# Performance work log

Hardware: AMD Instinct MI355X
Metric: run time of the kernel (lower is better)

Reference implementation:

```python
import jax, jax.numpy as jnp
import numpy as np

HEADS, BATCH, SEQ, CDIM = 8, 4, 2048, 32
WINDOW = 10

def setup_inputs() -> dict:
    key = jax.random.key(0)
    k1, k2, k3, k4 = jax.random.split(key, 4)
    shp = (HEADS, BATCH, SEQ, CDIM)
    return {
        'Q': jax.random.normal(k1, shp, dtype=jnp.float32),
        'K': jax.random.normal(k2, shp, dtype=jnp.float32),
        'V': jax.random.normal(k3, shp, dtype=jnp.float32),
        'G': jax.random.normal(k4, shp, dtype=jnp.float32),
        'seqMask': jnp.zeros((BATCH, SEQ), dtype=bool),  # no padded positions
    }

def reference(Q, K, V, G, seqMask):
    # Q,K,V,G: [h, n, s, c]; seqMask: [n, s] bool (True = masked key position)
    scale = 1.0 / jnp.sqrt(jnp.asarray(CDIM, dtype=Q.dtype))
    A = jnp.einsum('hnsi,hnti->hnst', Q, K) * scale  # [h,n,s,t]
    # padding mask on key axis
    A = jnp.where(seqMask[None, :, None, :], -jnp.inf, A)
    # local band mask |s-t| <= WINDOW (torch scatter construction clamps to
    # row bounds, which is equivalent to the plain band)
    idx = jnp.arange(SEQ)
    band = jnp.abs(idx[:, None] - idx[None, :]) <= WINDOW  # [s,t]
    A = jnp.where(band[None, None, :, :], A, -jnp.inf)
    A = jax.nn.softmax(A, axis=-1)
    # gated AV fusion: out[n,s,h,i] = sum_t A[h,n,s,t] V[h,n,t,i] * G[h,n,s,i]
    out = jnp.einsum('hnst,hnti,hnsi->nshi', A, V, G)
    return out
```

## Files before the change

### kernel.cpp

```cpp
#include <hip/hip_runtime.h>
#include <hip/hip_bf16.h>
#include <math.h>

#define HEADS 8
#define BATCH 4
#define SEQ 2048
#define CDIM 32
#define WINDOW 10

#define RPB 64
#define VROWS 96
#define VSTR 20

typedef float f32x4 __attribute__((ext_vector_type(4)));
typedef short s16x8 __attribute__((ext_vector_type(8)));
#define MFMA16 __builtin_amdgcn_mfma_f32_16x16x32_bf16

union BF8 { s16x8 v; __hip_bfloat162 h[4]; };
union U32 { __hip_bfloat162 h; unsigned u; };
union U4  { unsigned u[4]; s16x8 v; };

__global__ __launch_bounds__(256) void lwin_attn_kernel(
    const float* __restrict__ Q, const float* __restrict__ K,
    const float* __restrict__ V, const float* __restrict__ G,
    const unsigned char* __restrict__ seqMask, float* __restrict__ out)
{
    __shared__ unsigned V_s[VROWS * VSTR];

    const int d = blockIdx.x;
    const int b = (d & 7) * 128 + (d >> 3);

    const int hn = b >> 5;
    const int s0 = (b & 31) * RPB;
    const int n  = hn & 3;
    const int h  = hn >> 2;
    const int base_hn = hn * SEQ * CDIM;

    const int tid  = threadIdx.x;
    const int w    = tid >> 6;
    const int lane = tid & 63;
    const int q    = lane & 15;
    const int g    = lane >> 4;

    {
        const int i = tid >> 2, o = tid & 3;
        const int t  = s0 - 16 + i;
        const int tc = min(max(t, 0), SEQ - 1);
        const float4 f0 = *(const float4*)&V[base_hn + tc * 32 + 4 * o];
        const float4 f1 = *(const float4*)&V[base_hn + tc * 32 + 16 + 4 * o];
        U32 w0, w1, w2, w3;
        w0.h = __float22bfloat162_rn(make_float2(f0.x, f1.x));
        w1.h = __float22bfloat162_rn(make_float2(f0.y, f1.y));
        w2.h = __float22bfloat162_rn(make_float2(f0.z, f1.z));
        w3.h = __float22bfloat162_rn(make_float2(f0.w, f1.w));
        *(uint4*)&V_s[i * VSTR + 4 * o] = make_uint4(w0.u, w1.u, w2.u, w3.u);
    }
    if (tid < 128) {
        const int task = tid + 256;
        const int i = task >> 2, o = task & 3;
        const int t  = s0 - 16 + i;
        const int tc = min(max(t, 0), SEQ - 1);
        const float4 f0 = *(const float4*)&V[base_hn + tc * 32 + 4 * o];
        const float4 f1 = *(const float4*)&V[base_hn + tc * 32 + 16 + 4 * o];
        U32 w0, w1, w2, w3;
        w0.h = __float22bfloat162_rn(make_float2(f0.x, f1.x));
        w1.h = __float22bfloat162_rn(make_float2(f0.y, f1.y));
        w2.h = __float22bfloat162_rn(make_float2(f0.z, f1.z));
        w3.h = __float22bfloat162_rn(make_float2(f0.w, f1.w));
        *(uint4*)&V_s[i * VSTR + 4 * o] = make_uint4(w0.u, w1.u, w2.u, w3.u);
    }

    const int sw = s0 + 16 * w;

    const int rowq = hn * SEQ + sw + q;
    const float sc = 0.17677669529663687f * 1.4426950408889634f;
    const float4 q0 = *(const float4*)&Q[rowq * 32 + 8 * g];
    const float4 q1 = *(const float4*)&Q[rowq * 32 + 8 * g + 4];
    BF8 bq;
    bq.h[0] = __float22bfloat162_rn(make_float2(q0.x * sc, q0.y * sc));
    bq.h[1] = __float22bfloat162_rn(make_float2(q0.z * sc, q0.w * sc));
    bq.h[2] = __float22bfloat162_rn(make_float2(q1.x * sc, q1.y * sc));
    bq.h[3] = __float22bfloat162_rn(make_float2(q1.z * sc, q1.w * sc));
    const float4 g0 = *(const float4*)&G[rowq * 32 + 4 * g];
    const float4 g1 = *(const float4*)&G[rowq * 32 + 16 + 4 * g];

    BF8 ak[3];
#pragma unroll
    for (int blk = 0; blk < 3; ++blk) {
        const int t  = sw - 16 + 16 * blk + q;
        const int tc = min(max(t, 0), SEQ - 1);
        const float4 k0 = *(const float4*)&K[base_hn + tc * 32 + 8 * g];
        const float4 k1 = *(const float4*)&K[base_hn + tc * 32 + 8 * g + 4];
        ak[blk].h[0] = __float22bfloat162_rn(make_float2(k0.x, k0.y));
        ak[blk].h[1] = __float22bfloat162_rn(make_float2(k0.z, k0.w));
        ak[blk].h[2] = __float22bfloat162_rn(make_float2(k1.x, k1.y));
        ak[blk].h[3] = __float22bfloat162_rn(make_float2(k1.z, k1.w));
    }

    unsigned long long mI;
    {
        const int t  = sw - 16 + lane;
        const int tc = min(max(t, 0), SEQ - 1);
        const bool inval = (t < 0) || (t >= SEQ) || (seqMask[n * SEQ + tc] != 0);
        mI = __ballot(inval);
    }
    const unsigned long long vm = (0x1FFFFFULL << (q + 6)) & ~mI;

    f32x4 S[3];
#pragma unroll
    for (int blk = 0; blk < 3; ++blk)
        S[blk] = MFMA16(ak[blk].v, bq.v, (f32x4){0.f, 0.f, 0.f, 0.f}, 0, 0, 0);

    float sm = 0.f;
    unsigned pk[3][2];
#pragma unroll
    for (int blk = 0; blk < 3; ++blk) {
        float e[4];
#pragma unroll
        for (int r = 0; r < 4; ++r) {
            const int j = 16 * blk + 4 * g + r;
            const float x = ((vm >> j) & 1ULL) ? S[blk][r] : -1e30f;
            e[r] = __builtin_amdgcn_exp2f(x);
            sm += e[r];
        }
        U32 a, b2;
        a.h  = __float22bfloat162_rn(make_float2(e[0], e[1]));
        b2.h = __float22bfloat162_rn(make_float2(e[2], e[3]));
        pk[blk][0] = a.u;
        pk[blk][1] = b2.u;
    }
    sm += __shfl_xor(sm, 16);
    sm += __shfl_xor(sm, 32);

    __syncthreads();

    f32x4 O0 = {0.f, 0.f, 0.f, 0.f}, O1 = {0.f, 0.f, 0.f, 0.f};
    {
        const int R = 16 * w;
        unsigned r0[4], r1[4];
#pragma unroll
        for (int jj = 0; jj < 4; ++jj) {
            r0[jj] = V_s[(R + 4 * g + jj) * VSTR + q];
            r1[jj] = V_s[(R + 16 + 4 * g + jj) * VSTR + q];
        }
        U4 A0, A1v;
        A0.u[0]  = __builtin_amdgcn_perm(r0[1], r0[0], 0x05040100u);
        A0.u[1]  = __builtin_amdgcn_perm(r0[3], r0[2], 0x05040100u);
        A0.u[2]  = __builtin_amdgcn_perm(r1[1], r1[0], 0x05040100u);
        A0.u[3]  = __builtin_amdgcn_perm(r1[3], r1[2], 0x05040100u);
        A1v.u[0] = __builtin_amdgcn_perm(r0[1], r0[0], 0x07060302u);
        A1v.u[1] = __builtin_amdgcn_perm(r0[3], r0[2], 0x07060302u);
        A1v.u[2] = __builtin_amdgcn_perm(r1[1], r1[0], 0x07060302u);
        A1v.u[3] = __builtin_amdgcn_perm(r1[3], r1[2], 0x07060302u);
        U4 Bp;
        Bp.u[0] = pk[0][0]; Bp.u[1] = pk[0][1];
        Bp.u[2] = pk[1][0]; Bp.u[3] = pk[1][1];
        O0 = MFMA16(A0.v,  Bp.v, O0, 0, 0, 0);
        O1 = MFMA16(A1v.v, Bp.v, O1, 0, 0, 0);
    }
    {
        const int R = 16 * w + 32;
        unsigned r0[4];
#pragma unroll
        for (int jj = 0; jj < 4; ++jj)
            r0[jj] = V_s[(R + 4 * g + jj) * VSTR + q];
        U4 A0, A1v;
        A0.u[0]  = __builtin_amdgcn_perm(r0[1], r0[0], 0x05040100u);
        A0.u[1]  = __builtin_amdgcn_perm(r0[3], r0[2], 0x05040100u);
        A0.u[2]  = 0u; A0.u[3] = 0u;
        A1v.u[0] = __builtin_amdgcn_perm(r0[1], r0[0], 0x07060302u);
        A1v.u[1] = __builtin_amdgcn_perm(r0[3], r0[2], 0x07060302u);
        A1v.u[2] = 0u; A1v.u[3] = 0u;
        U4 Bp;
        Bp.u[0] = pk[2][0]; Bp.u[1] = pk[2][1];
        Bp.u[2] = 0u;       Bp.u[3] = 0u;
        O0 = MFMA16(A0.v,  Bp.v, O0, 0, 0, 0);
        O1 = MFMA16(A1v.v, Bp.v, O1, 0, 0, 0);
    }

    const float invq = 1.0f / sm;
    float4 o0, o1;
    o0.x = O0[0] * invq * g0.x;  o0.y = O0[1] * invq * g0.y;
    o0.z = O0[2] * invq * g0.z;  o0.w = O0[3] * invq * g0.w;
    o1.x = O1[0] * invq * g1.x;  o1.y = O1[1] * invq * g1.y;
    o1.z = O1[2] * invq * g1.z;  o1.w = O1[3] * invq * g1.w;
    float* obase = &out[((n * SEQ + sw + q) * HEADS + h) * 32];
    *(float4*)&obase[4 * g]      = o0;
    *(float4*)&obase[16 + 4 * g] = o1;
}

extern "C" void kernel_launch(void* const* d_in, const int* in_sizes, int n_in,
                              void* d_out, int out_size, void* d_ws, size_t ws_size,
                              hipStream_t stream) {
    const float* Q = (const float*)d_in[0];
    const float* K = (const float*)d_in[1];
    const float* V = (const float*)d_in[2];
    const float* G = (const float*)d_in[3];
    const unsigned char* seqMask = (const unsigned char*)d_in[4];
    float* out = (float*)d_out;

    const int blocks = HEADS * BATCH * (SEQ / RPB);
    lwin_attn_kernel<<<blocks, 256, 0, stream>>>(Q, K, V, G, seqMask, out);
}
```

Measured before the change: 14.17 us.

## Split channel halves across wave pairs and stage bf16 K in shared memory

Each block now covers 32 query rows instead of 64. Pairs of waves share one 16-row tile, and each wave computes one 16-channel half of the output, so the block count doubles and each wave does half the AV work. K is converted to bf16 once per block and staged in LDS, replacing the per-wave global loads of overlapping K windows. The trade-off is that QK^T and softmax are computed redundantly in both waves of a pair, and there is more halo overhead per block.

```diff
diff --git a/kernel.cpp b/kernel.cpp
--- a/kernel.cpp
+++ b/kernel.cpp
@@ -8,8 +8,8 @@
 #define CDIM 32
 #define WINDOW 10
 
-#define RPB 64
-#define VROWS 96
+#define RPB 32
+#define BROWS 64
 #define VSTR 20
 
 typedef float f32x4 __attribute__((ext_vector_type(4)));
@@ -25,19 +25,22 @@
     const float* __restrict__ V, const float* __restrict__ G,
     const unsigned char* __restrict__ seqMask, float* __restrict__ out)
 {
-    __shared__ unsigned V_s[VROWS * VSTR];
+    __shared__ short    K_s[BROWS * 32];
+    __shared__ unsigned V_s[BROWS * VSTR];
 
     const int d = blockIdx.x;
-    const int b = (d & 7) * 128 + (d >> 3);
+    const int b = (d & 7) * 256 + (d >> 3);
 
-    const int hn = b >> 5;
-    const int s0 = (b & 31) * RPB;
+    const int hn = b >> 6;
+    const int s0 = (b & 63) * RPB;
     const int n  = hn & 3;
     const int h  = hn >> 2;
     const int base_hn = hn * SEQ * CDIM;
 
     const int tid  = threadIdx.x;
-    const int w    = tid >> 6;
+    const int wave = tid >> 6;
+    const int tile = wave >> 1;
+    const int half = wave & 1;
     const int lane = tid & 63;
     const int q    = lane & 15;
     const int g    = lane >> 4;
@@ -46,22 +49,16 @@
         const int i = tid >> 2, o = tid & 3;
         const int t  = s0 - 16 + i;
         const int tc = min(max(t, 0), SEQ - 1);
+        const float4 k0 = *(const float4*)&K[base_hn + tc * 32 + 8 * o];
+        const float4 k1 = *(const float4*)&K[base_hn + tc * 32 + 8 * o + 4];
         const float4 f0 = *(const float4*)&V[base_hn + tc * 32 + 4 * o];
         const float4 f1 = *(const float4*)&V[base_hn + tc * 32 + 16 + 4 * o];
-        U32 w0, w1, w2, w3;
-        w0.h = __float22bfloat162_rn(make_float2(f0.x, f1.x));
-        w1.h = __float22bfloat162_rn(make_float2(f0.y, f1.y));
-        w2.h = __float22bfloat162_rn(make_float2(f0.z, f1.z));
-        w3.h = __float22bfloat162_rn(make_float2(f0.w, f1.w));
-        *(uint4*)&V_s[i * VSTR + 4 * o] = make_uint4(w0.u, w1.u, w2.u, w3.u);
-    }
-    if (tid < 128) {
-        const int task = tid + 256;
-        const int i = task >> 2, o = task & 3;
-        const int t  = s0 - 16 + i;
-        const int tc = min(max(t, 0), SEQ - 1);
-        const float4 f0 = *(const float4*)&V[base_hn + tc * 32 + 4 * o];
-        const float4 f1 = *(const float4*)&V[base_hn + tc * 32 + 16 + 4 * o];
+        BF8 uk;
+        uk.h[0] = __float22bfloat162_rn(make_float2(k0.x, k0.y));
+        uk.h[1] = __float22bfloat162_rn(make_float2(k0.z, k0.w));
+        uk.h[2] = __float22bfloat162_rn(make_float2(k1.x, k1.y));
+        uk.h[3] = __float22bfloat162_rn(make_float2(k1.z, k1.w));
+        *(s16x8*)&K_s[i * 32 + 8 * o] = uk.v;
         U32 w0, w1, w2, w3;
         w0.h = __float22bfloat162_rn(make_float2(f0.x, f1.x));
         w1.h = __float22bfloat162_rn(make_float2(f0.y, f1.y));
@@ -70,9 +67,9 @@
         *(uint4*)&V_s[i * VSTR + 4 * o] = make_uint4(w0.u, w1.u, w2.u, w3.u);
     }
 
-    const int sw = s0 + 16 * w;
+    const int sw   = s0 + 16 * tile;
+    const int rowq = hn * SEQ + sw + q;
 
-    const int rowq = hn * SEQ + sw + q;
     const float sc = 0.17677669529663687f * 1.4426950408889634f;
     const float4 q0 = *(const float4*)&Q[rowq * 32 + 8 * g];
     const float4 q1 = *(const float4*)&Q[rowq * 32 + 8 * g + 4];
@@ -81,21 +78,7 @@
     bq.h[1] = __float22bfloat162_rn(make_float2(q0.z * sc, q0.w * sc));
     bq.h[2] = __float22bfloat162_rn(make_float2(q1.x * sc, q1.y * sc));
     bq.h[3] = __float22bfloat162_rn(make_float2(q1.z * sc, q1.w * sc));
-    const float4 g0 = *(const float4*)&G[rowq * 32 + 4 * g];
-    const float4 g1 = *(const float4*)&G[rowq * 32 + 16 + 4 * g];
-
-    BF8 ak[3];
-#pragma unroll
-    for (int blk = 0; blk < 3; ++blk) {
-        const int t  = sw - 16 + 16 * blk + q;
-        const int tc = min(max(t, 0), SEQ - 1);
-        const float4 k0 = *(const float4*)&K[base_hn + tc * 32 + 8 * g];
-        const float4 k1 = *(const float4*)&K[base_hn + tc * 32 + 8 * g + 4];
-        ak[blk].h[0] = __float22bfloat162_rn(make_float2(k0.x, k0.y));
-        ak[blk].h[1] = __float22bfloat162_rn(make_float2(k0.z, k0.w));
-        ak[blk].h[2] = __float22bfloat162_rn(make_float2(k1.x, k1.y));
-        ak[blk].h[3] = __float22bfloat162_rn(make_float2(k1.z, k1.w));
-    }
+    const float4 gh = *(const float4*)&G[rowq * 32 + 16 * half + 4 * g];
 
     unsigned long long mI;
     {
@@ -106,10 +89,14 @@
     }
     const unsigned long long vm = (0x1FFFFFULL << (q + 6)) & ~mI;
 
+    __syncthreads();
+
     f32x4 S[3];
 #pragma unroll
-    for (int blk = 0; blk < 3; ++blk)
-        S[blk] = MFMA16(ak[blk].v, bq.v, (f32x4){0.f, 0.f, 0.f, 0.f}, 0, 0, 0);
+    for (int blk = 0; blk < 3; ++blk) {
+        const s16x8 ak = *(const s16x8*)&K_s[(16 * tile + 16 * blk + q) * 32 + 8 * g];
+        S[blk] = MFMA16(ak, bq.v, (f32x4){0.f, 0.f, 0.f, 0.f}, 0, 0, 0);
+    }
 
     float sm = 0.f;
     unsigned pk[3][2];
@@ -132,61 +119,47 @@
     sm += __shfl_xor(sm, 16);
     sm += __shfl_xor(sm, 32);
 
-    __syncthreads();
-
-    f32x4 O0 = {0.f, 0.f, 0.f, 0.f}, O1 = {0.f, 0.f, 0.f, 0.f};
+    const unsigned sel = half ? 0x07060302u : 0x05040100u;
+    f32x4 O = {0.f, 0.f, 0.f, 0.f};
     {
-        const int R = 16 * w;
+        const int R = 16 * tile;
         unsigned r0[4], r1[4];
 #pragma unroll
         for (int jj = 0; jj < 4; ++jj) {
             r0[jj] = V_s[(R + 4 * g + jj) * VSTR + q];
             r1[jj] = V_s[(R + 16 + 4 * g + jj) * VSTR + q];
         }
-        U4 A0, A1v;
-        A0.u[0]  = __builtin_amdgcn_perm(r0[1], r0[0], 0x05040100u);
-        A0.u[1]  = __builtin_amdgcn_perm(r0[3], r0[2], 0x05040100u);
-        A0.u[2]  = __builtin_amdgcn_perm(r1[1], r1[0], 0x05040100u);
-        A0.u[3]  = __builtin_amdgcn_perm(r1[3], r1[2], 0x05040100u);
-        A1v.u[0] = __builtin_amdgcn_perm(r0[1], r0[0], 0x07060302u);
-        A1v.u[1] = __builtin_amdgcn_perm(r0[3], r0[2], 0x07060302u);
-        A1v.u[2] = __builtin_amdgcn_perm(r1[1], r1[0], 0x07060302u);
-        A1v.u[3] = __builtin_amdgcn_perm(r1[3], r1[2], 0x07060302u);
+        U4 A;
+        A.u[0] = __builtin_amdgcn_perm(r0[1], r0[0], sel);
+        A.u[1] = __builtin_amdgcn_perm(r0[3], r0[2], sel);
+        A.u[2] = __builtin_amdgcn_perm(r1[1], r1[0], sel);
+        A.u[3] = __builtin_amdgcn_perm(r1[3], r1[2], sel);
         U4 Bp;
         Bp.u[0] = pk[0][0]; Bp.u[1] = pk[0][1];
         Bp.u[2] = pk[1][0]; Bp.u[3] = pk[1][1];
-        O0 = MFMA16(A0.v,  Bp.v, O0, 0, 0, 0);
-        O1 = MFMA16(A1v.v, Bp.v, O1, 0, 0, 0);
+        O = MFMA16(A.v, Bp.v, O, 0, 0, 0);
     }
     {
-        const int R = 16 * w + 32;
+        const int R = 16 * tile + 32;
         unsigned r0[4];
 #pragma unroll
         for (int jj = 0; jj < 4; ++jj)
             r0[jj] = V_s[(R + 4 * g + jj) * VSTR + q];
-        U4 A0, A1v;
-        A0.u[0]  = __builtin_amdgcn_perm(r0[1], r0[0], 0x05040100u);
-        A0.u[1]  = __builtin_amdgcn_perm(r0[3], r0[2], 0x05040100u);
-        A0.u[2]  = 0u; A0.u[3] = 0u;
-        A1v.u[0] = __builtin_amdgcn_perm(r0[1], r0[0], 0x07060302u);
-        A1v.u[1] = __builtin_amdgcn_perm(r0[3], r0[2], 0x07060302u);
-        A1v.u[2] = 0u; A1v.u[3] = 0u;
+        U4 A;
+        A.u[0] = __builtin_amdgcn_perm(r0[1], r0[0], sel);
+        A.u[1] = __builtin_amdgcn_perm(r0[3], r0[2], sel);
+        A.u[2] = 0u; A.u[3] = 0u;
         U4 Bp;
         Bp.u[0] = pk[2][0]; Bp.u[1] = pk[2][1];
         Bp.u[2] = 0u;       Bp.u[3] = 0u;
-        O0 = MFMA16(A0.v,  Bp.v, O0, 0, 0, 0);
-        O1 = MFMA16(A1v.v, Bp.v, O1, 0, 0, 0);
+        O = MFMA16(A.v, Bp.v, O, 0, 0, 0);
     }
 
     const float invq = 1.0f / sm;
-    float4 o0, o1;
-    o0.x = O0[0] * invq * g0.x;  o0.y = O0[1] * invq * g0.y;
-    o0.z = O0[2] * invq * g0.z;  o0.w = O0[3] * invq * g0.w;
-    o1.x = O1[0] * invq * g1.x;  o1.y = O1[1] * invq * g1.y;
-    o1.z = O1[2] * invq * g1.z;  o1.w = O1[3] * invq * g1.w;
-    float* obase = &out[((n * SEQ + sw + q) * HEADS + h) * 32];
-    *(float4*)&obase[4 * g]      = o0;
-    *(float4*)&obase[16 + 4 * g] = o1;
+    float4 o;
+    o.x = O[0] * invq * gh.x;  o.y = O[1] * invq * gh.y;
+    o.z = O[2] * invq * gh.z;  o.w = O[3] * invq * gh.w;
+    *(float4*)&out[((n * SEQ + sw + q) * HEADS + h) * 32 + 16 * half + 4 * g] = o;
 }
 
 extern "C" void kernel_launch(void* const* d_in, const int* in_sizes, int n_in,
```

After: 12.94 us. 8.7% less time.

## Process two 64-row phases per block with staged K/V shared-memory double buffering

Applied to the files above, without the earlier changes.

Each block now covers 128 query rows in two 64-row phases and is launched half as many times. All global loads for both phases (K, V, Q, G, mask) are issued up front into registers. K is also staged through shared memory in bf16, alongside V, in a double-buffered layout so phase two's commit can follow phase one's compute. The aim is to cut per-block launch overhead and hide global latency, at the cost of more registers, lower occupancy, and a still-redundant 32-row halo per phase.

```diff
diff --git a/kernel.cpp b/kernel.cpp
--- a/kernel.cpp
+++ b/kernel.cpp
@@ -8,8 +8,8 @@
 #define CDIM 32
 #define WINDOW 10
 
-#define RPB 64
-#define VROWS 96
+#define RPB 128
+#define PBAND 96
 #define VSTR 20
 
 typedef float f32x4 __attribute__((ext_vector_type(4)));
@@ -25,13 +25,14 @@
     const float* __restrict__ V, const float* __restrict__ G,
     const unsigned char* __restrict__ seqMask, float* __restrict__ out)
 {
-    __shared__ unsigned V_s[VROWS * VSTR];
+    __shared__ short    K_s[2][PBAND * 32];
+    __shared__ unsigned V_s[2][PBAND * VSTR];
 
     const int d = blockIdx.x;
-    const int b = (d & 7) * 128 + (d >> 3);
-
-    const int hn = b >> 5;
-    const int s0 = (b & 31) * RPB;
+    const int b = (d & 7) * 64 + (d >> 3);
+
+    const int hn = b >> 4;
+    const int s0 = (b & 15) * RPB;
     const int n  = hn & 3;
     const int h  = hn >> 2;
     const int base_hn = hn * SEQ * CDIM;
@@ -42,151 +43,166 @@
     const int q    = lane & 15;
     const int g    = lane >> 4;
 
-    {
-        const int i = tid >> 2, o = tid & 3;
-        const int t  = s0 - 16 + i;
-        const int tc = min(max(t, 0), SEQ - 1);
-        const float4 f0 = *(const float4*)&V[base_hn + tc * 32 + 4 * o];
-        const float4 f1 = *(const float4*)&V[base_hn + tc * 32 + 16 + 4 * o];
-        U32 w0, w1, w2, w3;
-        w0.h = __float22bfloat162_rn(make_float2(f0.x, f1.x));
-        w1.h = __float22bfloat162_rn(make_float2(f0.y, f1.y));
-        w2.h = __float22bfloat162_rn(make_float2(f0.z, f1.z));
-        w3.h = __float22bfloat162_rn(make_float2(f0.w, f1.w));
-        *(uint4*)&V_s[i * VSTR + 4 * o] = make_uint4(w0.u, w1.u, w2.u, w3.u);
+    float4 ld[2][3][2];
+#pragma unroll
+    for (int p = 0; p < 2; ++p) {
+        const int sp = s0 + 64 * p;
+#pragma unroll
+        for (int k = 0; k < 3; ++k) {
+            const int id = tid + 256 * k;
+            const bool isK = id < 384;
+            const int tt = isK ? id : id - 384;
+            const int i = tt >> 2, o = tt & 3;
+            const int t  = sp - 16 + i;
+            const int tc = min(max(t, 0), SEQ - 1);
+            const float* src = (isK ? K : V) + base_hn + tc * 32;
+            const int off0 = isK ? 8 * o : 4 * o;
+            const int off1 = isK ? 8 * o + 4 : 16 + 4 * o;
+            ld[p][k][0] = *(const float4*)&src[off0];
+            ld[p][k][1] = *(const float4*)&src[off1];
+        }
     }
-    if (tid < 128) {
-        const int task = tid + 256;
-        const int i = task >> 2, o = task & 3;
-        const int t  = s0 - 16 + i;
-        const int tc = min(max(t, 0), SEQ - 1);
-        const float4 f0 = *(const float4*)&V[base_hn + tc * 32 + 4 * o];
-        const float4 f1 = *(const float4*)&V[base_hn + tc * 32 + 16 + 4 * o];
-        U32 w0, w1, w2, w3;
-        w0.h = __float22bfloat162_rn(make_float2(f0.x, f1.x));
-        w1.h = __float22bfloat162_rn(make_float2(f0.y, f1.y));
-        w2.h = __float22bfloat162_rn(make_float2(f0.z, f1.z));
-        w3.h = __float22bfloat162_rn(make_float2(f0.w, f1.w));
-        *(uint4*)&V_s[i * VSTR + 4 * o] = make_uint4(w0.u, w1.u, w2.u, w3.u);
-    }
-
-    const int sw = s0 + 16 * w;
-
-    const int rowq = hn * SEQ + sw + q;
+
     const float sc = 0.17677669529663687f * 1.4426950408889634f;
-    const float4 q0 = *(const float4*)&Q[rowq * 32 + 8 * g];
-    const float4 q1 = *(const float4*)&Q[rowq * 32 + 8 * g + 4];
-    BF8 bq;
-    bq.h[0] = __float22bfloat162_rn(make_float2(q0.x * sc, q0.y * sc));
-    bq.h[1] = __float22bfloat162_rn(make_float2(q0.z * sc, q0.w * sc));
-    bq.h[2] = __float22bfloat162_rn(make_float2(q1.x * sc, q1.y * sc));
-    bq.h[3] = __float22bfloat162_rn(make_float2(q1.z * sc, q1.w * sc));
-    const float4 g0 = *(const float4*)&G[rowq * 32 + 4 * g];
-    const float4 g1 = *(const float4*)&G[rowq * 32 + 16 + 4 * g];
-
-    BF8 ak[3];
-#pragma unroll
-    for (int blk = 0; blk < 3; ++blk) {
-        const int t  = sw - 16 + 16 * blk + q;
-        const int tc = min(max(t, 0), SEQ - 1);
-        const float4 k0 = *(const float4*)&K[base_hn + tc * 32 + 8 * g];
-        const float4 k1 = *(const float4*)&K[base_hn + tc * 32 + 8 * g + 4];
-        ak[blk].h[0] = __float22bfloat162_rn(make_float2(k0.x, k0.y));
-        ak[blk].h[1] = __float22bfloat162_rn(make_float2(k0.z, k0.w));
-        ak[blk].h[2] = __float22bfloat162_rn(make_float2(k1.x, k1.y));
-        ak[blk].h[3] = __float22bfloat162_rn(make_float2(k1.z, k1.w));
-    }
-
-    unsigned long long mI;
-    {
+    BF8 bq[2];
+    float4 gA[2], gB[2];
+    unsigned long long mI[2];
+#pragma unroll
+    for (int p = 0; p < 2; ++p) {
+        const int sw   = s0 + 64 * p + 16 * w;
+        const int rowq = hn * SEQ + sw + q;
+        const float4 q0 = *(const float4*)&Q[rowq * 32 + 8 * g];
+        const float4 q1 = *(const float4*)&Q[rowq * 32 + 8 * g + 4];
+        bq[p].h[0] = __float22bfloat162_rn(make_float2(q0.x * sc, q0.y * sc));
+        bq[p].h[1] = __float22bfloat162_rn(make_float2(q0.z * sc, q0.w * sc));
+        bq[p].h[2] = __float22bfloat162_rn(make_float2(q1.x * sc, q1.y * sc));
+        bq[p].h[3] = __float22bfloat162_rn(make_float2(q1.z * sc, q1.w * sc));
+        gA[p] = *(const float4*)&G[rowq * 32 + 4 * g];
+        gB[p] = *(const float4*)&G[rowq * 32 + 16 + 4 * g];
         const int t  = sw - 16 + lane;
         const int tc = min(max(t, 0), SEQ - 1);
         const bool inval = (t < 0) || (t >= SEQ) || (seqMask[n * SEQ + tc] != 0);
-        mI = __ballot(inval);
+        mI[p] = __ballot(inval);
     }
-    const unsigned long long vm = (0x1FFFFFULL << (q + 6)) & ~mI;
-
-    f32x4 S[3];
-#pragma unroll
-    for (int blk = 0; blk < 3; ++blk)
-        S[blk] = MFMA16(ak[blk].v, bq.v, (f32x4){0.f, 0.f, 0.f, 0.f}, 0, 0, 0);
-
-    float sm = 0.f;
-    unsigned pk[3][2];
-#pragma unroll
-    for (int blk = 0; blk < 3; ++blk) {
-        float e[4];
-#pragma unroll
-        for (int r = 0; r < 4; ++r) {
-            const int j = 16 * blk + 4 * g + r;
-            const float x = ((vm >> j) & 1ULL) ? S[blk][r] : -1e30f;
-            e[r] = __builtin_amdgcn_exp2f(x);
-            sm += e[r];
-        }
-        U32 a, b2;
-        a.h  = __float22bfloat162_rn(make_float2(e[0], e[1]));
-        b2.h = __float22bfloat162_rn(make_float2(e[2], e[3]));
-        pk[blk][0] = a.u;
-        pk[blk][1] = b2.u;
-    }
-    sm += __shfl_xor(sm, 16);
-    sm += __shfl_xor(sm, 32);
-
+
+    auto commit = [&](const float4 (&L)[3][2], short* Ks, unsigned* Vs) {
+#pragma unroll
+        for (int k = 0; k < 3; ++k) {
+            const int id = tid + 256 * k;
+            const bool isK = id < 384;
+            const int tt = isK ? id : id - 384;
+            const int i = tt >> 2, o = tt & 3;
+            if (isK) {
+                BF8 u;
+                u.h[0] = __float22bfloat162_rn(make_float2(L[k][0].x, L[k][0].y));
+                u.h[1] = __float22bfloat162_rn(make_float2(L[k][0].z, L[k][0].w));
+                u.h[2] = __float22bfloat162_rn(make_float2(L[k][1].x, L[k][1].y));
+                u.h[3] = __float22bfloat162_rn(make_float2(L[k][1].z, L[k][1].w));
+                *(s16x8*)&Ks[i * 32 + 8 * o] = u.v;
+            } else {
+                U32 w0, w1, w2, w3;
+                w0.h = __float22bfloat162_rn(make_float2(L[k][0].x, L[k][1].x));
+                w1.h = __float22bfloat162_rn(make_float2(L[k][0].y, L[k][1].y));
+                w2.h = __float22bfloat162_rn(make_float2(L[k][0].z, L[k][1].z));
+                w3.h = __float22bfloat162_rn(make_float2(L[k][0].w, L[k][1].w));
+                *(uint4*)&Vs[i * VSTR + 4 * o] = make_uint4(w0.u, w1.u, w2.u, w3.u);
+            }
+        }
+    };
+
+    auto computePhase = [&](const short* Ks, const unsigned* Vs, int sp,
+                            const BF8& bqp, const float4& ga, const float4& gb,
+                            unsigned long long mIp) {
+        f32x4 S[3];
+#pragma unroll
+        for (int blk = 0; blk < 3; ++blk) {
+            const s16x8 ak = *(const s16x8*)&Ks[(16 * w + 16 * blk + q) * 32 + 8 * g];
+            S[blk] = MFMA16(ak, bqp.v, (f32x4){0.f, 0.f, 0.f, 0.f}, 0, 0, 0);
+        }
+        const unsigned long long vm = (0x1FFFFFULL << (q + 6)) & ~mIp;
+
+        float sm = 0.f;
+        unsigned pk[3][2];
+#pragma unroll
+        for (int blk = 0; blk < 3; ++blk) {
+            float e[4];
+#pragma unroll
+            for (int r = 0; r < 4; ++r) {
+                const int j = 16 * blk + 4 * g + r;
+                const float x = ((vm >> j) & 1ULL) ? S[blk][r] : -1e30f;
+                e[r] = __builtin_amdgcn_exp2f(x);
+                sm += e[r];
+            }
+            U32 a, b2;
+            a.h  = __float22bfloat162_rn(make_float2(e[0], e[1]));
+            b2.h = __float22bfloat162_rn(make_float2(e[2], e[3]));
+            pk[blk][0] = a.u;
+            pk[blk][1] = b2.u;
+        }
+        sm += __shfl_xor(sm, 16);
+        sm += __shfl_xor(sm, 32);
+
+        f32x4 O0 = {0.f, 0.f, 0.f, 0.f}, O1 = {0.f, 0.f, 0.f, 0.f};
+        {
+            const int R = 16 * w;
+            unsigned r0[4], r1[4];
+#pragma unroll
+            for (int jj = 0; jj < 4; ++jj) {
+                r0[jj] = Vs[(R + 4 * g + jj) * VSTR + q];
+                r1[jj] = Vs[(R + 16 + 4 * g + jj) * VSTR + q];
+            }
+            U4 A0, A1v;
+            A0.u[0]  = __builtin_amdgcn_perm(r0[1], r0[0], 0x05040100u);
+            A0.u[1]  = __builtin_amdgcn_perm(r0[3], r0[2], 0x05040100u);
+            A0.u[2]  = __builtin_amdgcn_perm(r1[1], r1[0], 0x05040100u);
+            A0.u[3]  = __builtin_amdgcn_perm(r1[3], r1[2], 0x05040100u);
+            A1v.u[0] = __builtin_amdgcn_perm(r0[1], r0[0], 0x07060302u);
+            A1v.u[1] = __builtin_amdgcn_perm(r0[3], r0[2], 0x07060302u);
+            A1v.u[2] = __builtin_amdgcn_perm(r1[1], r1[0], 0x07060302u);
+            A1v.u[3] = __builtin_amdgcn_perm(r1[3], r1[2], 0x07060302u);
+            U4 Bp;
+            Bp.u[0] = pk[0][0]; Bp.u[1] = pk[0][1];
+            Bp.u[2] = pk[1][0]; Bp.u[3] = pk[1][1];
+            O0 = MFMA16(A0.v,  Bp.v, O0, 0, 0, 0);
+            O1 = MFMA16(A1v.v, Bp.v, O1, 0, 0, 0);
+        }
+        {
+            const int R = 16 * w + 32;
+            unsigned r0[4];
+#pragma unroll
+            for (int jj = 0; jj < 4; ++jj)
+                r0[jj] = Vs[(R + 4 * g + jj) * VSTR + q];
+            U4 A0, A1v;
+            A0.u[0]  = __builtin_amdgcn_perm(r0[1], r0[0], 0x05040100u);
+            A0.u[1]  = __builtin_amdgcn_perm(r0[3], r0[2], 0x05040100u);
+            A0.u[2]  = 0u; A0.u[3] = 0u;
+            A1v.u[0] = __builtin_amdgcn_perm(r0[1], r0[0], 0x07060302u);
+            A1v.u[1] = __builtin_amdgcn_perm(r0[3], r0[2], 0x07060302u);
+            A1v.u[2] = 0u; A1v.u[3] = 0u;
+            U4 Bp;
+            Bp.u[0] = pk[2][0]; Bp.u[1] = pk[2][1];
+            Bp.u[2] = 0u;       Bp.u[3] = 0u;
+            O0 = MFMA16(A0.v,  Bp.v, O0, 0, 0, 0);
+            O1 = MFMA16(A1v.v, Bp.v, O1, 0, 0, 0);
+        }
+
+        const float invq = 1.0f / sm;
+        float4 o0, o1;
+        o0.x = O0[0] * invq * ga.x;  o0.y = O0[1] * invq * ga.y;
+        o0.z = O0[2] * invq * ga.z;  o0.w = O0[3] * invq * ga.w;
+        o1.x = O1[0] * invq * gb.x;  o1.y = O1[1] * invq * gb.y;
+        o1.z = O1[2] * invq * gb.z;  o1.w = O1[3] * invq * gb.w;
+        float* obase = &out[((n * SEQ + sp + 16 * w + q) * HEADS + h) * 32];
+        *(float4*)&obase[4 * g]      = o0;
+        *(float4*)&obase[16 + 4 * g] = o1;
+    };
+
+    commit(ld[0], K_s[0], V_s[0]);
     __syncthreads();
-
-    f32x4 O0 = {0.f, 0.f, 0.f, 0.f}, O1 = {0.f, 0.f, 0.f, 0.f};
-    {
-        const int R = 16 * w;
-        unsigned r0[4], r1[4];
-#pragma unroll
-        for (int jj = 0; jj < 4; ++jj) {
-            r0[jj] = V_s[(R + 4 * g + jj) * VSTR + q];
-            r1[jj] = V_s[(R + 16 + 4 * g + jj) * VSTR + q];
-        }
-        U4 A0, A1v;
-        A0.u[0]  = __builtin_amdgcn_perm(r0[1], r0[0], 0x05040100u);
-        A0.u[1]  = __builtin_amdgcn_perm(r0[3], r0[2], 0x05040100u);
-        A0.u[2]  = __builtin_amdgcn_perm(r1[1], r1[0], 0x05040100u);
-        A0.u[3]  = __builtin_amdgcn_perm(r1[3], r1[2], 0x05040100u);
-        A1v.u[0] = __builtin_amdgcn_perm(r0[1], r0[0], 0x07060302u);
-        A1v.u[1] = __builtin_amdgcn_perm(r0[3], r0[2], 0x07060302u);
-        A1v.u[2] = __builtin_amdgcn_perm(r1[1], r1[0], 0x07060302u);
-        A1v.u[3] = __builtin_amdgcn_perm(r1[3], r1[2], 0x07060302u);
-        U4 Bp;
-        Bp.u[0] = pk[0][0]; Bp.u[1] = pk[0][1];
-        Bp.u[2] = pk[1][0]; Bp.u[3] = pk[1][1];
-        O0 = MFMA16(A0.v,  Bp.v, O0, 0, 0, 0);
-        O1 = MFMA16(A1v.v, Bp.v, O1, 0, 0, 0);
-    }
-    {
-        const int R = 16 * w + 32;
-        unsigned r0[4];
-#pragma unroll
-        for (int jj = 0; jj < 4; ++jj)
-            r0[jj] = V_s[(R + 4 * g + jj) * VSTR + q];
-        U4 A0, A1v;
-        A0.u[0]  = __builtin_amdgcn_perm(r0[1], r0[0], 0x05040100u);
-        A0.u[1]  = __builtin_amdgcn_perm(r0[3], r0[2], 0x05040100u);
-        A0.u[2]  = 0u; A0.u[3] = 0u;
-        A1v.u[0] = __builtin_amdgcn_perm(r0[1], r0[0], 0x07060302u);
-        A1v.u[1] = __builtin_amdgcn_perm(r0[3], r0[2], 0x07060302u);
-        A1v.u[2] = 0u; A1v.u[3] = 0u;
-        U4 Bp;
-        Bp.u[0] = pk[2][0]; Bp.u[1] = pk[2][1];
-        Bp.u[2] = 0u;       Bp.u[3] = 0u;
-        O0 = MFMA16(A0.v,  Bp.v, O0, 0, 0, 0);
-        O1 = MFMA16(A1v.v, Bp.v, O1, 0, 0, 0);
-    }
-
-    const float invq = 1.0f / sm;
-    float4 o0, o1;
-    o0.x = O0[0] * invq * g0.x;  o0.y = O0[1] * invq * g0.y;
-    o0.z = O0[2] * invq * g0.z;  o0.w = O0[3] * invq * g0.w;
-    o1.x = O1[0] * invq * g1.x;  o1.y = O1[1] * invq * g1.y;
-    o1.z = O1[2] * invq * g1.z;  o1.w = O1[3] * invq * g1.w;
-    float* obase = &out[((n * SEQ + sw + q) * HEADS + h) * 32];
-    *(float4*)&obase[4 * g]      = o0;
-    *(float4*)&obase[16 + 4 * g] = o1;
+    computePhase(K_s[0], V_s[0], s0, bq[0], gA[0], gB[0], mI[0]);
+    commit(ld[1], K_s[1], V_s[1]);
+    __syncthreads();
+    computePhase(K_s[1], V_s[1], s0 + 64, bq[1], gA[1], gB[1], mI[1]);
 }
 
 extern "C" void kernel_launch(void* const* d_in, const int* in_sizes, int n_in,
```

New measurement: 13.20 us. 6.9% less time.

## Stage K and V per wave in shared memory and drop block barrier

Applied to the files above, without the earlier changes.

Each wave now loads its own 48-row K and V window into a private shared-memory slice instead of the block sharing one 96-row V tile. This removes the __syncthreads, since a wave only reads what it wrote itself. K is also staged through LDS, converted to bf16 once and then read back in the MFMA operand layout. All global loads are issued up front to raise memory-level parallelism. In exchange, overlapping halo rows are loaded redundantly (about 1.5x the V traffic plus extra K LDS writes), and shared memory use grows.

```diff
diff --git a/kernel.cpp b/kernel.cpp
--- a/kernel.cpp
+++ b/kernel.cpp
@@ -9,7 +9,7 @@
 #define WINDOW 10
 
 #define RPB 64
-#define VROWS 96
+#define WBAND 48
 #define VSTR 20
 
 typedef float f32x4 __attribute__((ext_vector_type(4)));
@@ -25,7 +25,8 @@
     const float* __restrict__ V, const float* __restrict__ G,
     const unsigned char* __restrict__ seqMask, float* __restrict__ out)
 {
-    __shared__ unsigned V_s[VROWS * VSTR];
+    __shared__ short    K_s[4][WBAND * 32];
+    __shared__ unsigned V_s[4][WBAND * VSTR];
 
     const int d = blockIdx.x;
     const int b = (d & 7) * 128 + (d >> 3);
@@ -42,60 +43,31 @@
     const int q    = lane & 15;
     const int g    = lane >> 4;
 
-    {
-        const int i = tid >> 2, o = tid & 3;
-        const int t  = s0 - 16 + i;
+    const int sw = s0 + 16 * w;
+    short*    Kw = K_s[w];
+    unsigned* Vw = V_s[w];
+
+    float4 kld[3][2], vld[3][2];
+#pragma unroll
+    for (int k = 0; k < 3; ++k) {
+        const int id = 64 * k + lane;
+        const int i  = id >> 2, o = id & 3;
+        const int t  = sw - 16 + i;
         const int tc = min(max(t, 0), SEQ - 1);
-        const float4 f0 = *(const float4*)&V[base_hn + tc * 32 + 4 * o];
-        const float4 f1 = *(const float4*)&V[base_hn + tc * 32 + 16 + 4 * o];
-        U32 w0, w1, w2, w3;
-        w0.h = __float22bfloat162_rn(make_float2(f0.x, f1.x));
-        w1.h = __float22bfloat162_rn(make_float2(f0.y, f1.y));
-        w2.h = __float22bfloat162_rn(make_float2(f0.z, f1.z));
-        w3.h = __float22bfloat162_rn(make_float2(f0.w, f1.w));
-        *(uint4*)&V_s[i * VSTR + 4 * o] = make_uint4(w0.u, w1.u, w2.u, w3.u);
+        const float* kb = K + base_hn + tc * 32;
+        const float* vb = V + base_hn + tc * 32;
+        kld[k][0] = *(const float4*)&kb[8 * o];
+        kld[k][1] = *(const float4*)&kb[8 * o + 4];
+        vld[k][0] = *(const float4*)&vb[4 * o];
+        vld[k][1] = *(const float4*)&vb[16 + 4 * o];
     }
-    if (tid < 128) {
-        const int task = tid + 256;
-        const int i = task >> 2, o = task & 3;
-        const int t  = s0 - 16 + i;
-        const int tc = min(max(t, 0), SEQ - 1);
-        const float4 f0 = *(const float4*)&V[base_hn + tc * 32 + 4 * o];
-        const float4 f1 = *(const float4*)&V[base_hn + tc * 32 + 16 + 4 * o];
-        U32 w0, w1, w2, w3;
-        w0.h = __float22bfloat162_rn(make_float2(f0.x, f1.x));
-        w1.h = __float22bfloat162_rn(make_float2(f0.y, f1.y));
-        w2.h = __float22bfloat162_rn(make_float2(f0.z, f1.z));
-        w3.h = __float22bfloat162_rn(make_float2(f0.w, f1.w));
-        *(uint4*)&V_s[i * VSTR + 4 * o] = make_uint4(w0.u, w1.u, w2.u, w3.u);
-    }
-
-    const int sw = s0 + 16 * w;
 
     const int rowq = hn * SEQ + sw + q;
     const float sc = 0.17677669529663687f * 1.4426950408889634f;
     const float4 q0 = *(const float4*)&Q[rowq * 32 + 8 * g];
     const float4 q1 = *(const float4*)&Q[rowq * 32 + 8 * g + 4];
-    BF8 bq;
-    bq.h[0] = __float22bfloat162_rn(make_float2(q0.x * sc, q0.y * sc));
-    bq.h[1] = __float22bfloat162_rn(make_float2(q0.z * sc, q0.w * sc));
-    bq.h[2] = __float22bfloat162_rn(make_float2(q1.x * sc, q1.y * sc));
-    bq.h[3] = __float22bfloat162_rn(make_float2(q1.z * sc, q1.w * sc));
-    const float4 g0 = *(const float4*)&G[rowq * 32 + 4 * g];
-    const float4 g1 = *(const float4*)&G[rowq * 32 + 16 + 4 * g];
-
-    BF8 ak[3];
-#pragma unroll
-    for (int blk = 0; blk < 3; ++blk) {
-        const int t  = sw - 16 + 16 * blk + q;
-        const int tc = min(max(t, 0), SEQ - 1);
-        const float4 k0 = *(const float4*)&K[base_hn + tc * 32 + 8 * g];
-        const float4 k1 = *(const float4*)&K[base_hn + tc * 32 + 8 * g + 4];
-        ak[blk].h[0] = __float22bfloat162_rn(make_float2(k0.x, k0.y));
-        ak[blk].h[1] = __float22bfloat162_rn(make_float2(k0.z, k0.w));
-        ak[blk].h[2] = __float22bfloat162_rn(make_float2(k1.x, k1.y));
-        ak[blk].h[3] = __float22bfloat162_rn(make_float2(k1.z, k1.w));
-    }
+    const float4 ga = *(const float4*)&G[rowq * 32 + 4 * g];
+    const float4 gb = *(const float4*)&G[rowq * 32 + 16 + 4 * g];
 
     unsigned long long mI;
     {
@@ -106,10 +78,36 @@
     }
     const unsigned long long vm = (0x1FFFFFULL << (q + 6)) & ~mI;
 
+    BF8 bq;
+    bq.h[0] = __float22bfloat162_rn(make_float2(q0.x * sc, q0.y * sc));
+    bq.h[1] = __float22bfloat162_rn(make_float2(q0.z * sc, q0.w * sc));
+    bq.h[2] = __float22bfloat162_rn(make_float2(q1.x * sc, q1.y * sc));
+    bq.h[3] = __float22bfloat162_rn(make_float2(q1.z * sc, q1.w * sc));
+
+#pragma unroll
+    for (int k = 0; k < 3; ++k) {
+        const int id = 64 * k + lane;
+        const int i  = id >> 2, o = id & 3;
+        BF8 uk;
+        uk.h[0] = __float22bfloat162_rn(make_float2(kld[k][0].x, kld[k][0].y));
+        uk.h[1] = __float22bfloat162_rn(make_float2(kld[k][0].z, kld[k][0].w));
+        uk.h[2] = __float22bfloat162_rn(make_float2(kld[k][1].x, kld[k][1].y));
+        uk.h[3] = __float22bfloat162_rn(make_float2(kld[k][1].z, kld[k][1].w));
+        *(s16x8*)&Kw[i * 32 + 8 * o] = uk.v;
+        U32 w0, w1, w2, w3;
+        w0.h = __float22bfloat162_rn(make_float2(vld[k][0].x, vld[k][1].x));
+        w1.h = __float22bfloat162_rn(make_float2(vld[k][0].y, vld[k][1].y));
+        w2.h = __float22bfloat162_rn(make_float2(vld[k][0].z, vld[k][1].z));
+        w3.h = __float22bfloat162_rn(make_float2(vld[k][0].w, vld[k][1].w));
+        *(uint4*)&Vw[i * VSTR + 4 * o] = make_uint4(w0.u, w1.u, w2.u, w3.u);
+    }
+
     f32x4 S[3];
 #pragma unroll
-    for (int blk = 0; blk < 3; ++blk)
-        S[blk] = MFMA16(ak[blk].v, bq.v, (f32x4){0.f, 0.f, 0.f, 0.f}, 0, 0, 0);
+    for (int blk = 0; blk < 3; ++blk) {
+        const s16x8 ak = *(const s16x8*)&Kw[(16 * blk + q) * 32 + 8 * g];
+        S[blk] = MFMA16(ak, bq.v, (f32x4){0.f, 0.f, 0.f, 0.f}, 0, 0, 0);
+    }
 
     float sm = 0.f;
     unsigned pk[3][2];
@@ -132,16 +130,13 @@
     sm += __shfl_xor(sm, 16);
     sm += __shfl_xor(sm, 32);
 
-    __syncthreads();
-
     f32x4 O0 = {0.f, 0.f, 0.f, 0.f}, O1 = {0.f, 0.f, 0.f, 0.f};
     {
-        const int R = 16 * w;
         unsigned r0[4], r1[4];
 #pragma unroll
         for (int jj = 0; jj < 4; ++jj) {
-            r0[jj] = V_s[(R + 4 * g + jj) * VSTR + q];
-            r1[jj] = V_s[(R + 16 + 4 * g + jj) * VSTR + q];
+            r0[jj] = Vw[(4 * g + jj) * VSTR + q];
+            r1[jj] = Vw[(16 + 4 * g + jj) * VSTR + q];
         }
         U4 A0, A1v;
         A0.u[0]  = __builtin_amdgcn_perm(r0[1], r0[0], 0x05040100u);
@@ -159,11 +154,10 @@
         O1 = MFMA16(A1v.v, Bp.v, O1, 0, 0, 0);
     }
     {
-        const int R = 16 * w + 32;
         unsigned r0[4];
 #pragma unroll
         for (int jj = 0; jj < 4; ++jj)
-            r0[jj] = V_s[(R + 4 * g + jj) * VSTR + q];
+            r0[jj] = Vw[(32 + 4 * g + jj) * VSTR + q];
         U4 A0, A1v;
         A0.u[0]  = __builtin_amdgcn_perm(r0[1], r0[0], 0x05040100u);
         A0.u[1]  = __builtin_amdgcn_perm(r0[3], r0[2], 0x05040100u);
@@ -180,10 +174,10 @@
 
     const float invq = 1.0f / sm;
     float4 o0, o1;
-    o0.x = O0[0] * invq * g0.x;  o0.y = O0[1] * invq * g0.y;
-    o0.z = O0[2] * invq * g0.z;  o0.w = O0[3] * invq * g0.w;
-    o1.x = O1[0] * invq * g1.x;  o1.y = O1[1] * invq * g1.y;
-    o1.z = O1[2] * invq * g1.z;  o1.w = O1[3] * invq * g1.w;
+    o0.x = O0[0] * invq * ga.x;  o0.y = O0[1] * invq * ga.y;
+    o0.z = O0[2] * invq * ga.z;  o0.w = O0[3] * invq * ga.w;
+    o1.x = O1[0] * invq * gb.x;  o1.y = O1[1] * invq * gb.y;
+    o1.z = O1[2] * invq * gb.z;  o1.w = O1[3] * invq * gb.w;
     float* obase = &out[((n * SEQ + sw + q) * HEADS + h) * 32];
     *(float4*)&obase[4 * g]      = o0;
     *(float4*)&obase[16 + 4 * g] = o1;
```

Result: faster. 12.72 us (-10.2%).
